# Performance work log

Measured on AMD Instinct MI355X. Metric: run time of the kernel, lower is better.

## Reference

```python
import jax, jax.numpy as jnp
import numpy as np

VOCAB = 50000
E = 300        # embedding_dim
HID = 512      # hidden_dim (bidirectional total)
HD = HID // 2  # per-direction hidden
K = 20         # tagset size
START = 18
STOP = 19
B = 64
T = 256
NEG = -10000.0


def setup_inputs() -> dict:
    key = jax.random.key(0)
    ks = jax.random.split(key, 12)
    s = 0.1
    sentence = jax.random.randint(ks[0], (B, T), 0, VOCAB)
    length = jax.random.randint(ks[1], (B,), T // 2, T + 1)
    embed_table = jax.random.normal(ks[2], (VOCAB, E)) * s
    w_ih_f = jax.random.normal(ks[3], (4 * HD, E)) * s
    w_hh_f = jax.random.normal(ks[4], (4 * HD, HD)) * s
    b_f = jax.random.normal(ks[5], (4 * HD,)) * s
    w_ih_b = jax.random.normal(ks[6], (4 * HD, E)) * s
    w_hh_b = jax.random.normal(ks[7], (4 * HD, HD)) * s
    b_b = jax.random.normal(ks[8], (4 * HD,)) * s
    W_out = jax.random.normal(ks[9], (K, HID)) * s
    b_out = jax.random.normal(ks[10], (K,)) * s
    transitions = jax.random.normal(ks[11], (K, K))
    transitions = transitions.at[START, :].set(NEG).at[:, STOP].set(NEG)
    return dict(sentence=sentence, length=length, embed_table=embed_table,
                w_ih_f=w_ih_f, w_hh_f=w_hh_f, b_f=b_f,
                w_ih_b=w_ih_b, w_hh_b=w_hh_b, b_b=b_b,
                W_out=W_out, b_out=b_out, transitions=transitions)


def _lstm(xs, w_ih, w_hh, b, reverse):
    # xs: [T, B, E]; PyTorch gate order i, f, g, o
    Bn = xs.shape[1]
    H = w_hh.shape[1]

    def step(carry, x):
        h, c = carry
        g = x @ w_ih.T + h @ w_hh.T + b
        i, f, gg, o = jnp.split(g, 4, axis=-1)
        c = jax.nn.sigmoid(f) * c + jax.nn.sigmoid(i) * jnp.tanh(gg)
        h = jax.nn.sigmoid(o) * jnp.tanh(c)
        return (h, c), h

    init = (jnp.zeros((Bn, H), xs.dtype), jnp.zeros((Bn, H), xs.dtype))
    _, hs = jax.lax.scan(step, init, xs, reverse=reverse)
    return hs  # [T, B, H], time-ordered


def _viterbi(feats, length, transitions):
    # feats: [B, T, K]; vectorized over batch, scan over time
    Bn, Tn, Kn = feats.shape
    fv0 = jnp.full((Bn, Kn), NEG, feats.dtype).at[:, START].set(0.0)
    idk = jnp.arange(Kn)

    def step(fv, inp):
        feat_t, t = inp
        # scores[b, next, prev] = fv[b, prev] + transitions[next, prev]
        sc = fv[:, None, :] + transitions[None, :, :]
        bp = jnp.argmax(sc, axis=-1)              # [B, K]
        best = jnp.max(sc, axis=-1) + feat_t      # [B, K]
        m = (t < length)[:, None]
        fv_new = jnp.where(m, best, fv)           # freeze past sentence end
        bp = jnp.where(m, bp, idk[None, :])       # identity backpointer on pad
        return fv_new, bp

    fv, bps = jax.lax.scan(step, fv0, (jnp.swapaxes(feats, 0, 1), jnp.arange(Tn)))
    term = fv + transitions[STOP][None, :]
    last = jnp.argmax(term, axis=-1)              # [B]
    score = jnp.max(term, axis=-1)                # [B] viterbi max score

    def back(tag, bp_t):
        prev = jnp.take_along_axis(bp_t, tag[:, None], axis=1)[:, 0]
        return prev, tag

    _, path_t = jax.lax.scan(back, last, bps, reverse=True)  # [T, B], time order
    path = jnp.swapaxes(path_t, 0, 1)             # [B, T]; entries >= length repeat last tag
    return score, path


def reference(sentence, length, embed_table, w_ih_f, w_hh_f, b_f,
              w_ih_b, w_hh_b, b_b, W_out, b_out, transitions):
    embeds = embed_table[sentence]                # [B, T, E]
    xs = jnp.swapaxes(embeds, 0, 1)               # [T, B, E]
    hf = _lstm(xs, w_ih_f, w_hh_f, b_f, reverse=False)
    hb = _lstm(xs, w_ih_b, w_hh_b, b_b, reverse=True)
    h = jnp.concatenate([hf, hb], axis=-1)        # [T, B, HID]
    feats = h @ W_out.T + b_out                   # [T, B, K]
    feats = jnp.swapaxes(feats, 0, 1)             # [B, T, K]
    score, path = _viterbi(feats, length, transitions)
    return score, path
```

## Files before the change

kernel.cpp:

```cpp
#include <hip/hip_runtime.h>
#include <hip/hip_bf16.h>

#define DINL __device__ __forceinline__

namespace {

typedef unsigned long long u64;

constexpr int Tn = 256;
constexpr int Bn = 64;
constexpr int HDn = 256;
constexpr int Kt = 20;
constexpr int STOPt = 19;
constexpr int STARTt = 18;
constexpr float NEGV = -10000.0f;

DINL float sigm(float x) { return 1.0f / (1.0f + __expf(-x)); }
DINL float tanh_f(float x) {
  float ax = fabsf(x);
  float e = __expf(-2.0f * ax);
  float t = (1.0f - e) / (1.0f + e);
  return x < 0.0f ? -t : t;
}

__global__ void k_epoch(unsigned* ep) {
  if (threadIdx.x == 0)
    __hip_atomic_fetch_add(ep, 1u, __ATOMIC_RELAXED, __HIP_MEMORY_SCOPE_AGENT);
}

__global__ void k_wt(const float* __restrict__ wf, const float* __restrict__ wb,
                     float* __restrict__ Wt) {
  int idx = blockIdx.x * 256 + threadIdx.x;
  if (idx >= 300 * 2048) return;
  int k = idx >> 11, n = idx & 2047;
  const float* w = (n < 1024) ? wf : wb;
  int nn = n & 1023;
  Wt[idx] = w[nn * 300 + k];
}

__global__ __launch_bounds__(256) void k_xproj(
    const int* __restrict__ sentence, const float* __restrict__ table,
    const float* __restrict__ Wt, const float* __restrict__ b_f,
    const float* __restrict__ b_b, float* __restrict__ xproj) {
  __shared__ float As[20][68];
  __shared__ float Bs[20][136];
  __shared__ int tok[64];

  int tid = threadIdx.x;
  int t = blockIdx.x;
  int n0 = blockIdx.y * 128;

  if (tid < 64) tok[tid] = sentence[tid * Tn + t];
  __syncthreads();

  int ty = tid >> 4, tx = tid & 15;
  float acc[4][8];
#pragma unroll
  for (int i = 0; i < 4; ++i)
#pragma unroll
    for (int j = 0; j < 8; ++j) acc[i][j] = 0.0f;

  for (int k0 = 0; k0 < 300; k0 += 20) {
#pragma unroll
    for (int i = 0; i < 5; ++i) {
      int idx = i * 256 + tid;
      int r = idx / 20, kk = idx % 20;
      As[kk][r] = table[tok[r] * 300 + k0 + kk];
    }
#pragma unroll
    for (int i = 0; i < 10; ++i) {
      int idx = i * 256 + tid;
      int kk = idx >> 7, c = idx & 127;
      Bs[kk][c] = Wt[(k0 + kk) * 2048 + n0 + c];
    }
    __syncthreads();
#pragma unroll
    for (int kk = 0; kk < 20; ++kk) {
      float4 a4 = *(const float4*)&As[kk][ty * 4];
      float4 b4a = *(const float4*)&Bs[kk][tx * 8];
      float4 b4b = *(const float4*)&Bs[kk][tx * 8 + 4];
      float av[4] = {a4.x, a4.y, a4.z, a4.w};
      float bvv[8] = {b4a.x, b4a.y, b4a.z, b4a.w, b4b.x, b4b.y, b4b.z, b4b.w};
#pragma unroll
      for (int i = 0; i < 4; ++i)
#pragma unroll
        for (int j = 0; j < 8; ++j) acc[i][j] += av[i] * bvv[j];
    }
    __syncthreads();
  }

  float bias[8];
#pragma unroll
  for (int j = 0; j < 8; ++j) {
    int n = n0 + tx * 8 + j;
    bias[j] = (n < 1024) ? b_f[n] : b_b[n - 1024];
  }
#pragma unroll
  for (int i = 0; i < 4; ++i) {
    size_t m = (size_t)t * 64 + ty * 4 + i;
    float* dst = &xproj[m * 2048 + n0 + tx * 8];
    float4 v0 = {acc[i][0] + bias[0], acc[i][1] + bias[1], acc[i][2] + bias[2],
                 acc[i][3] + bias[3]};
    float4 v1 = {acc[i][4] + bias[4], acc[i][5] + bias[5], acc[i][6] + bias[6],
                 acc[i][7] + bias[7]};
    *(float4*)dst = v0;
    *(float4*)(dst + 4) = v1;
  }
}

__global__ __launch_bounds__(128) void k_lstm(
    const float* __restrict__ whh_f, const float* __restrict__ whh_b,
    const float* __restrict__ xproj, float* __restrict__ h_all,
    int* __restrict__ flags, int* __restrict__ xcdtab,
    const unsigned* __restrict__ ep) {
  __shared__ __align__(16) float hl[16 * 256];
  __shared__ int fastsh;

  int tid = threadIdx.x;
  int bid = blockIdx.x;
  int gid = bid & 7;
  int s = bid >> 3;
  int dir = gid >> 2;
  int bg = gid & 3;
  const float* whh = dir ? whh_b : whh_f;

  int c = tid >> 4;
  int kc = tid & 15;

  unsigned E =
      __hip_atomic_load(ep, __ATOMIC_RELAXED, __HIP_MEMORY_SCOPE_AGENT);
  unsigned xcd = __builtin_amdgcn_s_getreg((3 << 11) | (0 << 6) | 20) & 0xFu;
  if (tid == 0) {
    __hip_atomic_store(&xcdtab[(gid << 5) + s],
                       (int)((E << 4) | xcd), __ATOMIC_RELAXED,
                       __HIP_MEMORY_SCOPE_AGENT);
  }
  if (tid < 64) {
    const int* xp_ = xcdtab + (gid << 5) + (tid & 31);
    unsigned v;
    for (;;) {
      v = (unsigned)__hip_atomic_load(xp_, __ATOMIC_RELAXED,
                                      __HIP_MEMORY_SCOPE_AGENT);
      bool rdy = (v >> 4) == (E & 0x0FFFFFFFu);
      if (__all((tid < 32) ? rdy : 1)) break;
      __builtin_amdgcn_s_sleep(1);
    }
    int mine = (int)(v & 0xFu);
    int ref = __shfl(mine, 0, 64);
    bool eq = (mine == ref);
    bool alleq = __all((tid < 32) ? eq : 1);
    if (tid == 0) fastsh = alleq ? 1 : 0;
  }

  float4 w4[4][4];
#pragma unroll
  for (int g = 0; g < 4; ++g) {
    const float* src = whh + ((size_t)(g * 256 + s * 8 + c)) * 256;
#pragma unroll
    for (int jj = 0; jj < 4; ++jj)
      w4[g][jj] = *(const float4*)(src + ((kc + (jj << 4)) << 2));
  }

  __syncthreads();
  const bool fast = (fastsh != 0);
  const unsigned base = E * 256u;

  float c_reg = 0.0f;

  for (int st = 0; st < Tn; ++st) {
    int xt = dir ? (Tn - 1 - st) : st;

    float xp[4];
    {
      size_t xb = ((size_t)(xt * 64 + bg * 16 + kc)) * 2048 + dir * 1024 +
                  s * 8 + c;
#pragma unroll
      for (int g = 0; g < 4; ++g)
        xp[g] = __builtin_nontemporal_load(&xproj[xb + g * 256]);
    }

    float acc[16][4];
#pragma unroll
    for (int b = 0; b < 16; ++b)
#pragma unroll
      for (int g = 0; g < 4; ++g) acc[b][g] = 0.0f;

    if (st > 0) {
      if (tid < 64) {
        const int* fp = flags + ((gid << 5) + (tid & 31)) * 4;
        if (fast) {
          for (;;) {
            unsigned v = (unsigned)__hip_atomic_load(
                fp, __ATOMIC_RELAXED, __HIP_MEMORY_SCOPE_AGENT);
            int d = (int)(v - base);
            if (__all((tid < 32) ? (d >= st) : 1)) break;
          }
        } else {
          for (;;) {
            unsigned v = (unsigned)__hip_atomic_load(
                fp, __ATOMIC_RELAXED, __HIP_MEMORY_SCOPE_AGENT);
            int d = (int)(v - base);
            if (__all((tid < 32) ? (d >= st) : 1)) break;
            __builtin_amdgcn_s_sleep(1);
          }
        }
      }
      __syncthreads();

      int pt = dir ? (xt + 1) : (xt - 1);
      const float* hsrc =
          h_all + ((size_t)(dir * Tn + pt) * 64 + bg * 16) * 256;
      const char* tb = (const char*)hsrc + (size_t)tid * 16;
      const char* p0 = tb;
      const char* p1 = tb + 4096;
      const char* p2 = tb + 8192;
      const char* p3 = tb + 12288;
      float4 q0, q1, q2, q3, q4, q5, q6, q7;
      asm volatile(
          "global_load_dwordx4 %0, %8, off sc1\n\t"
          "global_load_dwordx4 %1, %8, off offset:2048 sc1\n\t"
          "global_load_dwordx4 %2, %9, off sc1\n\t"
          "global_load_dwordx4 %3, %9, off offset:2048 sc1\n\t"
          "global_load_dwordx4 %4, %10, off sc1\n\t"
          "global_load_dwordx4 %5, %10, off offset:2048 sc1\n\t"
          "global_load_dwordx4 %6, %11, off sc1\n\t"
          "global_load_dwordx4 %7, %11, off offset:2048 sc1\n\t"
          "s_waitcnt vmcnt(0)"
          : "=&v"(q0), "=&v"(q1), "=&v"(q2), "=&v"(q3), "=&v"(q4), "=&v"(q5),
            "=&v"(q6), "=&v"(q7)
          : "v"(p0), "v"(p1), "v"(p2), "v"(p3));
      *(float4*)&hl[(tid + 0 * 128) << 2] = q0;
      *(float4*)&hl[(tid + 1 * 128) << 2] = q1;
      *(float4*)&hl[(tid + 2 * 128) << 2] = q2;
      *(float4*)&hl[(tid + 3 * 128) << 2] = q3;
      *(float4*)&hl[(tid + 4 * 128) << 2] = q4;
      *(float4*)&hl[(tid + 5 * 128) << 2] = q5;
      *(float4*)&hl[(tid + 6 * 128) << 2] = q6;
      *(float4*)&hl[(tid + 7 * 128) << 2] = q7;
      __syncthreads();

#pragma unroll
      for (int b = 0; b < 16; ++b) {
#pragma unroll
        for (int jj = 0; jj < 4; ++jj) {
          float4 hv = *(const float4*)&hl[b * 256 + ((kc + (jj << 4)) << 2)];
#pragma unroll
          for (int g = 0; g < 4; ++g) {
            acc[b][g] += w4[g][jj].x * hv.x + w4[g][jj].y * hv.y +
                         w4[g][jj].z * hv.z + w4[g][jj].w * hv.w;
          }
        }
      }
    }

#pragma unroll
    for (int r = 0; r < 4; ++r) {
      int m = 1 << r;
      int kb = (kc >> r) & 1;
#pragma unroll
      for (int ii = 0; ii < (16 >> (r + 1)); ++ii) {
#pragma unroll
        for (int g = 0; g < 4; ++g) {
          float e = acc[2 * ii][g], o = acc[2 * ii + 1][g];
          float kept = kb ? o : e;
          float sent = kb ? e : o;
          acc[ii][g] = kept + __shfl_xor(sent, m, 64);
        }
      }
    }

    {
      float gi = acc[0][0] + xp[0];
      float gf = acc[0][1] + xp[1];
      float gg = acc[0][2] + xp[2];
      float go = acc[0][3] + xp[3];
      c_reg = sigm(gf) * c_reg + sigm(gi) * tanh_f(gg);
      float h = sigm(go) * tanh_f(c_reg);
      size_t hi = ((size_t)(dir * Tn + xt) * 64 + bg * 16 + kc) * 256 + s * 8 +
                  c;
      if (fast) {
        h_all[hi] = h;
      } else {
        __hip_atomic_store(&h_all[hi], h, __ATOMIC_RELAXED,
                           __HIP_MEMORY_SCOPE_AGENT);
      }
    }

    asm volatile("s_waitcnt vmcnt(0)" ::: "memory");
    __syncthreads();
    if (tid == 0) {
      int fv = (int)(base + (unsigned)(st + 1));
      if (fast) {
        flags[((gid << 5) + s) * 4] = fv;
      } else {
        __hip_atomic_store(flags + ((gid << 5) + s) * 4, fv, __ATOMIC_RELAXED,
                           __HIP_MEMORY_SCOPE_AGENT);
      }
    }
  }
}

__global__ __launch_bounds__(256) void k_feats(const float* __restrict__ h_all,
                                               const float* __restrict__ Wout,
                                               const float* __restrict__ bout,
                                               float* __restrict__ feats) {
  __shared__ float Wl[20 * 512];
  __shared__ float hlf[64 * 256];

  int tid = threadIdx.x;
  int t = blockIdx.x;
  for (int i = tid; i < 20 * 512; i += 256) Wl[i] = Wout[i];

  float acc[5] = {0, 0, 0, 0, 0};
  int b = tid & 63, kg5 = tid >> 6;
  int swz = b & 7;

  for (int d = 0; d < 2; ++d) {
    __syncthreads();
    const float* hsrc = h_all + ((size_t)(d * Tn + t)) * 64 * 256;
#pragma unroll 8
    for (int i = 0; i < 64; ++i) {
      int idx = i * 256 + tid;
      int hb = idx >> 8, k = idx & 255;
      hlf[hb * 256 + 4 * ((k >> 2) ^ (hb & 7)) + (k & 3)] = hsrc[idx];
    }
    __syncthreads();
    for (int jg = 0; jg < 64; ++jg) {
      float4 hv = *(const float4*)&hlf[b * 256 + 4 * (jg ^ swz)];
#pragma unroll
      for (int kk = 0; kk < 5; ++kk) {
        int krow = kg5 * 5 + kk;
        float4 wvv = *(const float4*)&Wl[krow * 512 + d * 256 + jg * 4];
        acc[kk] += hv.x * wvv.x + hv.y * wvv.y + hv.z * wvv.z + hv.w * wvv.w;
      }
    }
  }
#pragma unroll
  for (int kk = 0; kk < 5; ++kk) {
    int krow = kg5 * 5 + kk;
    feats[((size_t)b * Tn + t) * Kt + krow] = acc[kk] + bout[krow];
  }
}

__global__ __launch_bounds__(64) void k_viterbi(const float* __restrict__ feats,
                                                const float* __restrict__ trans,
                                                const int* __restrict__ length,
                                                float* __restrict__ out) {
  __shared__ float tr[400];
  __shared__ float fv[20];
  __shared__ float term[20];
  __shared__ unsigned char bps[256][20];

  int b = blockIdx.x;
  int lane = threadIdx.x;
  for (int i = lane; i < 400; i += 64) tr[i] = trans[i];
  if (lane < 20) fv[lane] = (lane == STARTt) ? 0.0f : NEGV;
  int len = length[b];
  __syncthreads();

  for (int t = 0; t < Tn; ++t) {
    float nf = 0.0f;
    int bp = 0;
    if (lane < 20) {
      if (t < len) {
        float vmax = -3.4e38f;
        int pb = 0;
#pragma unroll
        for (int p = 0; p < 20; ++p) {
          float v = fv[p] + tr[lane * 20 + p];
          if (v > vmax) { vmax = v; pb = p; }
        }
        nf = vmax + feats[((size_t)b * Tn + t) * Kt + lane];
        bp = pb;
      } else {
        nf = fv[lane];
        bp = lane;
      }
    }
    __syncthreads();
    if (lane < 20) {
      fv[lane] = nf;
      bps[t][lane] = (unsigned char)bp;
    }
    __syncthreads();
  }

  if (lane < 20) term[lane] = fv[lane] + tr[STOPt * 20 + lane];
  __syncthreads();
  if (lane == 0) {
    float smax = term[0];
    int last = 0;
    for (int p = 1; p < 20; ++p)
      if (term[p] > smax) { smax = term[p]; last = p; }
    out[b] = smax;
    int tag = last;
    for (int t = Tn - 1; t >= 0; --t) {
      out[64 + b * Tn + t] = (float)tag;
      tag = bps[t][tag];
    }
  }
}

}

extern "C" void kernel_launch(void* const* d_in, const int* in_sizes, int n_in,
                              void* d_out, int out_size, void* d_ws,
                              size_t ws_size, hipStream_t stream) {
  const int* sentence = (const int*)d_in[0];
  const int* length = (const int*)d_in[1];
  const float* table = (const float*)d_in[2];
  const float* w_ih_f = (const float*)d_in[3];
  const float* w_hh_f = (const float*)d_in[4];
  const float* b_f = (const float*)d_in[5];
  const float* w_ih_b = (const float*)d_in[6];
  const float* w_hh_b = (const float*)d_in[7];
  const float* b_b = (const float*)d_in[8];
  const float* W_out = (const float*)d_in[9];
  const float* b_out = (const float*)d_in[10];
  const float* trans = (const float*)d_in[11];
  float* out = (float*)d_out;

  float* ws = (float*)d_ws;
  float* xproj = ws;
  float* h_all = ws + (size_t)33554432;
  float* Wt = h_all + (size_t)8388608;
  float* feats = Wt + (size_t)300 * 2048;
  int* flags = (int*)(feats + (size_t)Bn * Tn * Kt);
  int* xcdtab = flags + 1024;
  unsigned* ep = (unsigned*)(xcdtab + 256);
  (void)ws_size; (void)in_sizes; (void)n_in; (void)out_size;

  k_epoch<<<dim3(1), dim3(64), 0, stream>>>(ep);
  k_wt<<<dim3(2400), dim3(256), 0, stream>>>(w_ih_f, w_ih_b, Wt);
  k_xproj<<<dim3(256, 16), dim3(256), 0, stream>>>(sentence, table, Wt, b_f,
                                                   b_b, xproj);
  k_lstm<<<dim3(256), dim3(128), 0, stream>>>(w_hh_f, w_hh_b, xproj, h_all,
                                              flags, xcdtab, ep);
  k_feats<<<dim3(256), dim3(256), 0, stream>>>(h_all, W_out, b_out, feats);
  k_viterbi<<<dim3(64), dim3(64), 0, stream>>>(feats, trans, length, out);
}
```

Baseline: 1.485 ms.

## Fuse input projection into LSTM kernel with per-timestep producer/consumer counters

Merges the embedding-gather input projection GEMM and the recurrent LSTM into one launch. Extra worker blocks compute the projection for each timestep, ordered so both directions are served early, and bump a per-timestep counter once their stores are visible. The recurrent blocks spin on that counter before reading each step's projection. This overlaps the projection GEMM with the serial recurrence. It relies on all 512 blocks being co-resident and adds atomic-store and polling overhead.

```diff
diff --git a/kernel.cpp b/kernel.cpp
--- a/kernel.cpp
+++ b/kernel.cpp
@@ -23,7 +23,15 @@
   return x < 0.0f ? -t : t;
 }
 
-__global__ void k_epoch(unsigned* ep) {
+DINL void agent_st64(u64* p, u64 v) {
+  __hip_atomic_store(p, v, __ATOMIC_RELAXED, __HIP_MEMORY_SCOPE_AGENT);
+}
+DINL u64 pack2(float a, float b) {
+  return (u64)__float_as_uint(a) | ((u64)__float_as_uint(b) << 32);
+}
+
+__global__ void k_init(int* cnt, unsigned* ep) {
+  if (threadIdx.x < 256) cnt[threadIdx.x] = 0;
   if (threadIdx.x == 0)
     __hip_atomic_fetch_add(ep, 1u, __ATOMIC_RELAXED, __HIP_MEMORY_SCOPE_AGENT);
 }
@@ -38,86 +46,104 @@
   Wt[idx] = w[nn * 300 + k];
 }
 
-__global__ __launch_bounds__(256) void k_xproj(
+__global__ __launch_bounds__(128) void k_fused(
+    const float* __restrict__ whh_f, const float* __restrict__ whh_b,
     const int* __restrict__ sentence, const float* __restrict__ table,
     const float* __restrict__ Wt, const float* __restrict__ b_f,
-    const float* __restrict__ b_b, float* __restrict__ xproj) {
-  __shared__ float As[20][68];
-  __shared__ float Bs[20][136];
-  __shared__ int tok[64];
-
-  int tid = threadIdx.x;
-  int t = blockIdx.x;
-  int n0 = blockIdx.y * 128;
-
-  if (tid < 64) tok[tid] = sentence[tid * Tn + t];
-  __syncthreads();
-
-  int ty = tid >> 4, tx = tid & 15;
-  float acc[4][8];
-#pragma unroll
-  for (int i = 0; i < 4; ++i)
-#pragma unroll
-    for (int j = 0; j < 8; ++j) acc[i][j] = 0.0f;
-
-  for (int k0 = 0; k0 < 300; k0 += 20) {
-#pragma unroll
-    for (int i = 0; i < 5; ++i) {
-      int idx = i * 256 + tid;
-      int r = idx / 20, kk = idx % 20;
-      As[kk][r] = table[tok[r] * 300 + k0 + kk];
-    }
-#pragma unroll
-    for (int i = 0; i < 10; ++i) {
-      int idx = i * 256 + tid;
-      int kk = idx >> 7, c = idx & 127;
-      Bs[kk][c] = Wt[(k0 + kk) * 2048 + n0 + c];
-    }
-    __syncthreads();
-#pragma unroll
-    for (int kk = 0; kk < 20; ++kk) {
-      float4 a4 = *(const float4*)&As[kk][ty * 4];
-      float4 b4a = *(const float4*)&Bs[kk][tx * 8];
-      float4 b4b = *(const float4*)&Bs[kk][tx * 8 + 4];
-      float av[4] = {a4.x, a4.y, a4.z, a4.w};
-      float bvv[8] = {b4a.x, b4a.y, b4a.z, b4a.w, b4b.x, b4b.y, b4b.z, b4b.w};
-#pragma unroll
-      for (int i = 0; i < 4; ++i)
-#pragma unroll
-        for (int j = 0; j < 8; ++j) acc[i][j] += av[i] * bvv[j];
-    }
-    __syncthreads();
-  }
-
-  float bias[8];
-#pragma unroll
-  for (int j = 0; j < 8; ++j) {
-    int n = n0 + tx * 8 + j;
-    bias[j] = (n < 1024) ? b_f[n] : b_b[n - 1024];
-  }
-#pragma unroll
-  for (int i = 0; i < 4; ++i) {
-    size_t m = (size_t)t * 64 + ty * 4 + i;
-    float* dst = &xproj[m * 2048 + n0 + tx * 8];
-    float4 v0 = {acc[i][0] + bias[0], acc[i][1] + bias[1], acc[i][2] + bias[2],
-                 acc[i][3] + bias[3]};
-    float4 v1 = {acc[i][4] + bias[4], acc[i][5] + bias[5], acc[i][6] + bias[6],
-                 acc[i][7] + bias[7]};
-    *(float4*)dst = v0;
-    *(float4*)(dst + 4) = v1;
-  }
-}
-
-__global__ __launch_bounds__(128) void k_lstm(
-    const float* __restrict__ whh_f, const float* __restrict__ whh_b,
-    const float* __restrict__ xproj, float* __restrict__ h_all,
-    int* __restrict__ flags, int* __restrict__ xcdtab,
-    const unsigned* __restrict__ ep) {
-  __shared__ __align__(16) float hl[16 * 256];
+    const float* __restrict__ b_b, float* __restrict__ xproj,
+    float* __restrict__ h_all, int* __restrict__ flags,
+    int* __restrict__ xcdtab, const unsigned* __restrict__ ep,
+    int* __restrict__ cnt) {
+  __shared__ __align__(16) float shbuf[4160];
   __shared__ int fastsh;
 
   int tid = threadIdx.x;
   int bid = blockIdx.x;
+
+  if (bid >= 256) {
+    int w = bid - 256;
+    float(*As)[68] = (float(*)[68])shbuf;
+    float(*Bs)[136] = (float(*)[136])(shbuf + 20 * 68);
+    int* tok = (int*)(shbuf + 20 * 68 + 20 * 136);
+    int ty = tid >> 3, tx = tid & 7;
+
+    for (int it = 0; it < 16; ++it) {
+      int tau = w + (it << 8);
+      int tseq = tau >> 4, strip = tau & 15;
+      int t = (tseq & 1) ? (255 - (tseq >> 1)) : (tseq >> 1);
+      int n0 = strip << 7;
+
+      if (tid < 64) tok[tid] = sentence[tid * Tn + t];
+      __syncthreads();
+
+      float acc[4][16];
+#pragma unroll
+      for (int i = 0; i < 4; ++i)
+#pragma unroll
+        for (int j = 0; j < 16; ++j) acc[i][j] = 0.0f;
+
+      for (int k0 = 0; k0 < 300; k0 += 20) {
+#pragma unroll
+        for (int i = 0; i < 10; ++i) {
+          int idx = i * 128 + tid;
+          int r = idx / 20, kk = idx % 20;
+          As[kk][r] = table[tok[r] * 300 + k0 + kk];
+        }
+#pragma unroll
+        for (int i = 0; i < 20; ++i) {
+          int idx = i * 128 + tid;
+          int kk = idx >> 7, cc = idx & 127;
+          Bs[kk][cc] = Wt[(k0 + kk) * 2048 + n0 + cc];
+        }
+        __syncthreads();
+#pragma unroll
+        for (int kk = 0; kk < 20; ++kk) {
+          float4 a4 = *(const float4*)&As[kk][ty * 4];
+          float av[4] = {a4.x, a4.y, a4.z, a4.w};
+          float4 b4[4];
+#pragma unroll
+          for (int j4 = 0; j4 < 4; ++j4)
+            b4[j4] = *(const float4*)&Bs[kk][tx * 16 + j4 * 4];
+#pragma unroll
+          for (int i = 0; i < 4; ++i)
+#pragma unroll
+            for (int j4 = 0; j4 < 4; ++j4) {
+              acc[i][j4 * 4 + 0] += av[i] * b4[j4].x;
+              acc[i][j4 * 4 + 1] += av[i] * b4[j4].y;
+              acc[i][j4 * 4 + 2] += av[i] * b4[j4].z;
+              acc[i][j4 * 4 + 3] += av[i] * b4[j4].w;
+            }
+        }
+        __syncthreads();
+      }
+
+      const float* bb = (n0 < 1024) ? (b_f + n0) : (b_b + (n0 - 1024));
+      float bv[16];
+#pragma unroll
+      for (int j = 0; j < 16; ++j) bv[j] = bb[tx * 16 + j];
+#pragma unroll
+      for (int i = 0; i < 4; ++i) {
+        size_t m = (size_t)t * 64 + ty * 4 + i;
+        u64* dst = (u64*)&xproj[m * 2048 + n0 + tx * 16];
+#pragma unroll
+        for (int j = 0; j < 8; ++j) {
+          agent_st64(dst + j,
+                     pack2(acc[i][2 * j] + bv[2 * j],
+                           acc[i][2 * j + 1] + bv[2 * j + 1]));
+        }
+      }
+      asm volatile("s_waitcnt vmcnt(0)" ::: "memory");
+      __syncthreads();
+      if (tid == 0)
+        __hip_atomic_fetch_add(&cnt[t], 1, __ATOMIC_RELAXED,
+                               __HIP_MEMORY_SCOPE_AGENT);
+      __syncthreads();
+    }
+    return;
+  }
+
+  float* hl = shbuf;
+
   int gid = bid & 7;
   int s = bid >> 3;
   int dir = gid >> 2;
@@ -131,9 +157,8 @@
       __hip_atomic_load(ep, __ATOMIC_RELAXED, __HIP_MEMORY_SCOPE_AGENT);
   unsigned xcd = __builtin_amdgcn_s_getreg((3 << 11) | (0 << 6) | 20) & 0xFu;
   if (tid == 0) {
-    __hip_atomic_store(&xcdtab[(gid << 5) + s],
-                       (int)((E << 4) | xcd), __ATOMIC_RELAXED,
-                       __HIP_MEMORY_SCOPE_AGENT);
+    __hip_atomic_store(&xcdtab[(gid << 5) + s], (int)((E << 4) | xcd),
+                       __ATOMIC_RELAXED, __HIP_MEMORY_SCOPE_AGENT);
   }
   if (tid < 64) {
     const int* xp_ = xcdtab + (gid << 5) + (tid & 31);
@@ -169,6 +194,17 @@
 
   for (int st = 0; st < Tn; ++st) {
     int xt = dir ? (Tn - 1 - st) : st;
+
+    {
+      const int* cp = cnt + xt;
+      for (;;) {
+        int v = __hip_atomic_load(cp, __ATOMIC_RELAXED,
+                                  __HIP_MEMORY_SCOPE_AGENT);
+        if (v >= 16) break;
+        __builtin_amdgcn_s_sleep(2);
+      }
+      asm volatile("" ::: "memory");
+    }
 
     float xp[4];
     {
@@ -428,14 +464,14 @@
   int* flags = (int*)(feats + (size_t)Bn * Tn * Kt);
   int* xcdtab = flags + 1024;
   unsigned* ep = (unsigned*)(xcdtab + 256);
+  int* cnt = (int*)(ep + 1);
   (void)ws_size; (void)in_sizes; (void)n_in; (void)out_size;
 
-  k_epoch<<<dim3(1), dim3(64), 0, stream>>>(ep);
+  k_init<<<dim3(1), dim3(256), 0, stream>>>(cnt, ep);
   k_wt<<<dim3(2400), dim3(256), 0, stream>>>(w_ih_f, w_ih_b, Wt);
-  k_xproj<<<dim3(256, 16), dim3(256), 0, stream>>>(sentence, table, Wt, b_f,
-                                                   b_b, xproj);
-  k_lstm<<<dim3(256), dim3(128), 0, stream>>>(w_hh_f, w_hh_b, xproj, h_all,
-                                              flags, xcdtab, ep);
+  k_fused<<<dim3(512), dim3(128), 0, stream>>>(w_hh_f, w_hh_b, sentence, table,
+                                               Wt, b_f, b_b, xproj, h_all,
+                                               flags, xcdtab, ep, cnt);
   k_feats<<<dim3(256), dim3(256), 0, stream>>>(h_all, W_out, b_out, feats);
   k_viterbi<<<dim3(64), dim3(64), 0, stream>>>(feats, trans, length, out);
 }
```

Result: slower. 1.693 ms (+14.0%).

## Fuse embedding gather and input projection into the recurrent LSTM kernel

Applied to the files above, without the earlier changes.

Removes the separate weight-transpose and input-projection GEMM kernels and the 128MB xproj buffer. Each LSTM block now holds its slice of W_ih in shared memory and double-buffers gathered embedding rows per step, computing the input contribution inside the time loop before waiting on the flags. This saves the large global write and re-read plus two launches. In exchange it adds per-step FMA work on the serial critical path and a large shared-memory footprint per block.

```diff
diff --git a/kernel.cpp b/kernel.cpp
--- a/kernel.cpp
+++ b/kernel.cpp
@@ -28,92 +28,16 @@
     __hip_atomic_fetch_add(ep, 1u, __ATOMIC_RELAXED, __HIP_MEMORY_SCOPE_AGENT);
 }
 
-__global__ void k_wt(const float* __restrict__ wf, const float* __restrict__ wb,
-                     float* __restrict__ Wt) {
-  int idx = blockIdx.x * 256 + threadIdx.x;
-  if (idx >= 300 * 2048) return;
-  int k = idx >> 11, n = idx & 2047;
-  const float* w = (n < 1024) ? wf : wb;
-  int nn = n & 1023;
-  Wt[idx] = w[nn * 300 + k];
-}
-
-__global__ __launch_bounds__(256) void k_xproj(
-    const int* __restrict__ sentence, const float* __restrict__ table,
-    const float* __restrict__ Wt, const float* __restrict__ b_f,
-    const float* __restrict__ b_b, float* __restrict__ xproj) {
-  __shared__ float As[20][68];
-  __shared__ float Bs[20][136];
-  __shared__ int tok[64];
-
-  int tid = threadIdx.x;
-  int t = blockIdx.x;
-  int n0 = blockIdx.y * 128;
-
-  if (tid < 64) tok[tid] = sentence[tid * Tn + t];
-  __syncthreads();
-
-  int ty = tid >> 4, tx = tid & 15;
-  float acc[4][8];
-#pragma unroll
-  for (int i = 0; i < 4; ++i)
-#pragma unroll
-    for (int j = 0; j < 8; ++j) acc[i][j] = 0.0f;
-
-  for (int k0 = 0; k0 < 300; k0 += 20) {
-#pragma unroll
-    for (int i = 0; i < 5; ++i) {
-      int idx = i * 256 + tid;
-      int r = idx / 20, kk = idx % 20;
-      As[kk][r] = table[tok[r] * 300 + k0 + kk];
-    }
-#pragma unroll
-    for (int i = 0; i < 10; ++i) {
-      int idx = i * 256 + tid;
-      int kk = idx >> 7, c = idx & 127;
-      Bs[kk][c] = Wt[(k0 + kk) * 2048 + n0 + c];
-    }
-    __syncthreads();
-#pragma unroll
-    for (int kk = 0; kk < 20; ++kk) {
-      float4 a4 = *(const float4*)&As[kk][ty * 4];
-      float4 b4a = *(const float4*)&Bs[kk][tx * 8];
-      float4 b4b = *(const float4*)&Bs[kk][tx * 8 + 4];
-      float av[4] = {a4.x, a4.y, a4.z, a4.w};
-      float bvv[8] = {b4a.x, b4a.y, b4a.z, b4a.w, b4b.x, b4b.y, b4b.z, b4b.w};
-#pragma unroll
-      for (int i = 0; i < 4; ++i)
-#pragma unroll
-        for (int j = 0; j < 8; ++j) acc[i][j] += av[i] * bvv[j];
-    }
-    __syncthreads();
-  }
-
-  float bias[8];
-#pragma unroll
-  for (int j = 0; j < 8; ++j) {
-    int n = n0 + tx * 8 + j;
-    bias[j] = (n < 1024) ? b_f[n] : b_b[n - 1024];
-  }
-#pragma unroll
-  for (int i = 0; i < 4; ++i) {
-    size_t m = (size_t)t * 64 + ty * 4 + i;
-    float* dst = &xproj[m * 2048 + n0 + tx * 8];
-    float4 v0 = {acc[i][0] + bias[0], acc[i][1] + bias[1], acc[i][2] + bias[2],
-                 acc[i][3] + bias[3]};
-    float4 v1 = {acc[i][4] + bias[4], acc[i][5] + bias[5], acc[i][6] + bias[6],
-                 acc[i][7] + bias[7]};
-    *(float4*)dst = v0;
-    *(float4*)(dst + 4) = v1;
-  }
-}
-
 __global__ __launch_bounds__(128) void k_lstm(
     const float* __restrict__ whh_f, const float* __restrict__ whh_b,
-    const float* __restrict__ xproj, float* __restrict__ h_all,
-    int* __restrict__ flags, int* __restrict__ xcdtab,
-    const unsigned* __restrict__ ep) {
+    const float* __restrict__ wih_f, const float* __restrict__ wih_b,
+    const float* __restrict__ b_f, const float* __restrict__ b_b,
+    const int* __restrict__ sentence, const float* __restrict__ table,
+    float* __restrict__ h_all, int* __restrict__ flags,
+    int* __restrict__ xcdtab, const unsigned* __restrict__ ep) {
   __shared__ __align__(16) float hl[16 * 256];
+  __shared__ __align__(16) float embs[2][16 * 320];
+  __shared__ __align__(16) float wihs[32 * 324];
   __shared__ int fastsh;
 
   int tid = threadIdx.x;
@@ -123,6 +47,7 @@
   int dir = gid >> 2;
   int bg = gid & 3;
   const float* whh = dir ? whh_b : whh_f;
+  const float* wih = dir ? wih_b : wih_f;
 
   int c = tid >> 4;
   int kc = tid & 15;
@@ -131,9 +56,8 @@
       __hip_atomic_load(ep, __ATOMIC_RELAXED, __HIP_MEMORY_SCOPE_AGENT);
   unsigned xcd = __builtin_amdgcn_s_getreg((3 << 11) | (0 << 6) | 20) & 0xFu;
   if (tid == 0) {
-    __hip_atomic_store(&xcdtab[(gid << 5) + s],
-                       (int)((E << 4) | xcd), __ATOMIC_RELAXED,
-                       __HIP_MEMORY_SCOPE_AGENT);
+    __hip_atomic_store(&xcdtab[(gid << 5) + s], (int)((E << 4) | xcd),
+                       __ATOMIC_RELAXED, __HIP_MEMORY_SCOPE_AGENT);
   }
   if (tid < 64) {
     const int* xp_ = xcdtab + (gid << 5) + (tid & 31);
@@ -152,6 +76,16 @@
     if (tid == 0) fastsh = alleq ? 1 : 0;
   }
 
+  for (int i = tid; i < 32 * 81; i += 128) {
+    int r = i / 81, gi = i - r * 81;
+    int g = r >> 3, cc = r & 7;
+    float4 v = {0.0f, 0.0f, 0.0f, 0.0f};
+    if (gi < 75)
+      v = *(const float4*)(wih + ((size_t)(g * 256 + s * 8 + cc)) * 300 +
+                           4 * gi);
+    *(float4*)&wihs[r * 324 + 4 * gi] = v;
+  }
+
   float4 w4[4][4];
 #pragma unroll
   for (int g = 0; g < 4; ++g) {
@@ -161,6 +95,25 @@
       w4[g][jj] = *(const float4*)(src + ((kc + (jj << 4)) << 2));
   }
 
+  float bias4[4];
+  {
+    const float* bsrc = dir ? b_b : b_f;
+#pragma unroll
+    for (int g = 0; g < 4; ++g) bias4[g] = bsrc[g * 256 + s * 8 + c];
+  }
+
+  {
+    int xt0 = dir ? (Tn - 1) : 0;
+    int row = tid >> 3, j8 = tid & 7;
+    int tk = sentence[(bg * 16 + row) * Tn + xt0];
+#pragma unroll
+    for (int jj = 0; jj < 10; ++jj) {
+      int gi = j8 + 8 * jj;
+      float4 v = {0.0f, 0.0f, 0.0f, 0.0f};
+      if (gi < 75) v = *(const float4*)(table + (size_t)tk * 300 + 4 * gi);
+      *(float4*)&embs[0][row * 320 + 4 * gi] = v;
+    }
+  }
   __syncthreads();
   const bool fast = (fastsh != 0);
   const unsigned base = E * 256u;
@@ -169,21 +122,31 @@
 
   for (int st = 0; st < Tn; ++st) {
     int xt = dir ? (Tn - 1 - st) : st;
-
-    float xp[4];
-    {
-      size_t xb = ((size_t)(xt * 64 + bg * 16 + kc)) * 2048 + dir * 1024 +
-                  s * 8 + c;
-#pragma unroll
-      for (int g = 0; g < 4; ++g)
-        xp[g] = __builtin_nontemporal_load(&xproj[xb + g * 256]);
-    }
+    int eb = st & 1;
+    const float* emb = embs[eb];
 
     float acc[16][4];
 #pragma unroll
     for (int b = 0; b < 16; ++b)
 #pragma unroll
       for (int g = 0; g < 4; ++g) acc[b][g] = 0.0f;
+
+#pragma unroll
+    for (int jj = 0; jj < 5; ++jj) {
+      int gq = (kc + (jj << 4)) << 2;
+      float4 wv0 = *(const float4*)&wihs[(0 * 8 + c) * 324 + gq];
+      float4 wv1 = *(const float4*)&wihs[(1 * 8 + c) * 324 + gq];
+      float4 wv2 = *(const float4*)&wihs[(2 * 8 + c) * 324 + gq];
+      float4 wv3 = *(const float4*)&wihs[(3 * 8 + c) * 324 + gq];
+#pragma unroll
+      for (int b = 0; b < 16; ++b) {
+        float4 ev = *(const float4*)&emb[b * 320 + gq];
+        acc[b][0] += wv0.x * ev.x + wv0.y * ev.y + wv0.z * ev.z + wv0.w * ev.w;
+        acc[b][1] += wv1.x * ev.x + wv1.y * ev.y + wv1.z * ev.z + wv1.w * ev.w;
+        acc[b][2] += wv2.x * ev.x + wv2.y * ev.y + wv2.z * ev.z + wv2.w * ev.w;
+        acc[b][3] += wv3.x * ev.x + wv3.y * ev.y + wv3.z * ev.z + wv3.w * ev.w;
+      }
+    }
 
     if (st > 0) {
       if (tid < 64) {
@@ -270,10 +233,10 @@
     }
 
     {
-      float gi = acc[0][0] + xp[0];
-      float gf = acc[0][1] + xp[1];
-      float gg = acc[0][2] + xp[2];
-      float go = acc[0][3] + xp[3];
+      float gi = acc[0][0] + bias4[0];
+      float gf = acc[0][1] + bias4[1];
+      float gg = acc[0][2] + bias4[2];
+      float go = acc[0][3] + bias4[3];
       c_reg = sigm(gf) * c_reg + sigm(gi) * tanh_f(gg);
       float h = sigm(go) * tanh_f(c_reg);
       size_t hi = ((size_t)(dir * Tn + xt) * 64 + bg * 16 + kc) * 256 + s * 8 +
@@ -283,6 +246,20 @@
       } else {
         __hip_atomic_store(&h_all[hi], h, __ATOMIC_RELAXED,
                            __HIP_MEMORY_SCOPE_AGENT);
+      }
+    }
+
+    if (st + 1 < Tn) {
+      int xtn = dir ? (Tn - 2 - st) : (st + 1);
+      int row = tid >> 3, j8 = tid & 7;
+      int tk = sentence[(bg * 16 + row) * Tn + xtn];
+      float* ed = embs[eb ^ 1];
+#pragma unroll
+      for (int jj = 0; jj < 10; ++jj) {
+        int gi = j8 + 8 * jj;
+        float4 v = {0.0f, 0.0f, 0.0f, 0.0f};
+        if (gi < 75) v = *(const float4*)(table + (size_t)tk * 300 + 4 * gi);
+        *(float4*)&ed[row * 320 + 4 * gi] = v;
       }
     }
 
@@ -421,20 +398,16 @@
   float* out = (float*)d_out;
 
   float* ws = (float*)d_ws;
-  float* xproj = ws;
-  float* h_all = ws + (size_t)33554432;
-  float* Wt = h_all + (size_t)8388608;
-  float* feats = Wt + (size_t)300 * 2048;
+  float* h_all = ws;
+  float* feats = h_all + (size_t)8388608;
   int* flags = (int*)(feats + (size_t)Bn * Tn * Kt);
   int* xcdtab = flags + 1024;
   unsigned* ep = (unsigned*)(xcdtab + 256);
   (void)ws_size; (void)in_sizes; (void)n_in; (void)out_size;
 
   k_epoch<<<dim3(1), dim3(64), 0, stream>>>(ep);
-  k_wt<<<dim3(2400), dim3(256), 0, stream>>>(w_ih_f, w_ih_b, Wt);
-  k_xproj<<<dim3(256, 16), dim3(256), 0, stream>>>(sentence, table, Wt, b_f,
-                                                   b_b, xproj);
-  k_lstm<<<dim3(256), dim3(128), 0, stream>>>(w_hh_f, w_hh_b, xproj, h_all,
+  k_lstm<<<dim3(256), dim3(128), 0, stream>>>(w_hh_f, w_hh_b, w_ih_f, w_ih_b,
+                                              b_f, b_b, sentence, table, h_all,
                                               flags, xcdtab, ep);
   k_feats<<<dim3(256), dim3(256), 0, stream>>>(h_all, W_out, b_out, feats);
   k_viterbi<<<dim3(64), dim3(64), 0, stream>>>(feats, trans, length, out);
```

After: 2.072 ms. 1.4x slower.
